# Kernel optimization log

Hardware: AMD Instinct MI355X
Metric: run time of the kernel (lower is better)

## Reference

```python
import jax, jax.numpy as jnp
import numpy as np

N_PARTICLES = 512
N_DIMS = 3
EPS_LJ = 1.0
RM = 1.0
ENERGY_FACTOR = 1.0
OSC_SCALE = 1.0
DIST_EPS = 1e-6  # bgflow distances_from_vectors eps inside sqrt


def setup_inputs() -> dict:
    key = jax.random.key(0)
    x = jax.random.normal(key, (128, N_PARTICLES * N_DIMS), dtype=jnp.float32)
    return {"x": x}


def reference(x):
    B = x.shape[0]
    xp = x.reshape(B, N_PARTICLES, N_DIMS)
    # all-pairs distance vectors r_ij = x_i - x_j  -> [B, N, N, D]
    diff = xp[:, :, None, :] - xp[:, None, :, :]
    r = jnp.sqrt(jnp.sum(diff * diff, axis=-1) + DIST_EPS)  # [B, N, N]
    eye = jnp.eye(N_PARTICLES, dtype=bool)
    # mask diagonal (bgflow removes self-pairs before the LJ energy)
    r_safe = jnp.where(eye, 1.0, r)
    inv6 = (RM / r_safe) ** 6
    lj = EPS_LJ * (inv6 * inv6 - 2.0 * inv6)
    lj = jnp.where(eye, 0.0, lj)
    lj_energies = lj.reshape(B, -1).sum(axis=-1) * ENERGY_FACTOR
    # harmonic oscillator term on mean-centered coordinates
    xc = xp - jnp.mean(xp, axis=1, keepdims=True)
    osc = 0.5 * jnp.sum(xc * xc, axis=(-2, -1))
    total = lj_energies + osc * OSC_SCALE
    return total[:, None]
```

## Files before the change

kernel.cpp:

```cpp
#include <hip/hip_runtime.h>

#define NP 512
#define BLOCK 512
#define JW 64
constexpr float DIST_EPS = 1e-6f;

__device__ __forceinline__ float waveSum(float v) {
    v += __shfl_down(v, 32, 64);
    v += __shfl_down(v, 16, 64);
    v += __shfl_down(v, 8, 64);
    v += __shfl_down(v, 4, 64);
    v += __shfl_down(v, 2, 64);
    v += __shfl_down(v, 1, 64);
    return v;
}

__global__ __launch_bounds__(BLOCK, 8) void lj_kernel(const float* __restrict__ x,
                                                      float* __restrict__ out) {
    const int b   = blockIdx.x >> 3;
    const int q   = blockIdx.x & 7;
    const int tid = threadIdx.x;
    const float* __restrict__ xb = x + b * (NP * 3);

    __shared__ __align__(16) float s[3 * NP];
    __shared__ float red[8 * 5];

    for (int g = tid; g < 3 * NP; g += BLOCK) {
        float v = xb[g];
        int p = g / 3;
        int d = g - p * 3;
        s[d * NP + p] = v;
    }
    __syncthreads();

    const float* sx = s;
    const float* sy = s + NP;
    const float* sz = s + 2 * NP;

    const int i     = tid;
    const int jbase = q * JW;

    const float xi = sx[i], yi = sy[i], zi = sz[i];

    float a0 = 0.f, a1 = 0.f, a2 = 0.f, a3 = 0.f;

    #pragma unroll 2
    for (int j = jbase; j < jbase + JW; j += 4) {
        float4 jx = *reinterpret_cast<const float4*>(sx + j);
        float4 jy = *reinterpret_cast<const float4*>(sy + j);
        float4 jz = *reinterpret_cast<const float4*>(sz + j);

        {
            float dx = xi - jx.x, dy = yi - jy.x, dz = zi - jz.x;
            float d2 = fmaf(dx, dx, fmaf(dy, dy, fmaf(dz, dz, DIST_EPS)));
            float d6 = d2 * d2 * d2;
            float i6 = __builtin_amdgcn_rcpf(d6);
            i6 = (j + 0 == i) ? 0.f : i6;
            a0 = fmaf(i6, i6 - 2.0f, a0);
        }
        {
            float dx = xi - jx.y, dy = yi - jy.y, dz = zi - jz.y;
            float d2 = fmaf(dx, dx, fmaf(dy, dy, fmaf(dz, dz, DIST_EPS)));
            float d6 = d2 * d2 * d2;
            float i6 = __builtin_amdgcn_rcpf(d6);
            i6 = (j + 1 == i) ? 0.f : i6;
            a1 = fmaf(i6, i6 - 2.0f, a1);
        }
        {
            float dx = xi - jx.z, dy = yi - jy.z, dz = zi - jz.z;
            float d2 = fmaf(dx, dx, fmaf(dy, dy, fmaf(dz, dz, DIST_EPS)));
            float d6 = d2 * d2 * d2;
            float i6 = __builtin_amdgcn_rcpf(d6);
            i6 = (j + 2 == i) ? 0.f : i6;
            a2 = fmaf(i6, i6 - 2.0f, a2);
        }
        {
            float dx = xi - jx.w, dy = yi - jy.w, dz = zi - jz.w;
            float d2 = fmaf(dx, dx, fmaf(dy, dy, fmaf(dz, dz, DIST_EPS)));
            float d6 = d2 * d2 * d2;
            float i6 = __builtin_amdgcn_rcpf(d6);
            i6 = (j + 3 == i) ? 0.f : i6;
            a3 = fmaf(i6, i6 - 2.0f, a3);
        }
    }
    float acc = (a0 + a1) + (a2 + a3);

    float sxs = 0.f, sys = 0.f, szs = 0.f, sqs = 0.f;
    if (q == 0) {
        float px = sx[tid], py = sy[tid], pz = sz[tid];
        sxs = px; sys = py; szs = pz;
        sqs = fmaf(px, px, fmaf(py, py, pz * pz));
    }

    const int wid  = tid >> 6;
    const int lane = tid & 63;
    float r0 = waveSum(acc);
    float r1 = waveSum(sxs);
    float r2 = waveSum(sys);
    float r3 = waveSum(szs);
    float r4 = waveSum(sqs);
    if (lane == 0) {
        red[wid * 5 + 0] = r0;
        red[wid * 5 + 1] = r1;
        red[wid * 5 + 2] = r2;
        red[wid * 5 + 3] = r3;
        red[wid * 5 + 4] = r4;
    }
    __syncthreads();
    if (tid == 0) {
        float t0 = 0.f, t1 = 0.f, t2 = 0.f, t3 = 0.f, t4 = 0.f;
        #pragma unroll
        for (int w = 0; w < 8; ++w) {
            t0 += red[w * 5 + 0];
            t1 += red[w * 5 + 1];
            t2 += red[w * 5 + 2];
            t3 += red[w * 5 + 3];
            t4 += red[w * 5 + 4];
        }
        float total = t0;
        if (q == 0) {
            float m2 = (t1 * t1 + t2 * t2 + t3 * t3) * (1.0f / NP);
            total += 0.5f * (t4 - m2);
        }
        atomicAdd(out + b, total);
    }
}

extern "C" void kernel_launch(void* const* d_in, const int* in_sizes, int n_in,
                              void* d_out, int out_size, void* d_ws, size_t ws_size,
                              hipStream_t stream) {
    const float* x = (const float*)d_in[0];
    float* out = (float*)d_out;
    const int B = in_sizes[0] / (NP * 3);
    lj_kernel<<<dim3(8 * B, 1, 1), BLOCK, 0, stream>>>(x, out);
}
```

Measured before the change: 65.08 us.

## Exploit pair symmetry to halve LJ pair evaluations via circular half-window

Uses the symmetry of the pair energy to compute each unordered pair once. Particle coordinates are duplicated into shared memory so each thread can walk a wrapped window of about half the particles, and the block sum is doubled. Boundary groups get special handling: a partial first group (j > i), and half weights on the antipodal group. The diagonal masks leave the inner loop, so the remaining arithmetic is roughly halved, at the cost of more shared memory, extra edge code, and uneven work across the q blocks.

```diff
diff --git a/kernel.cpp b/kernel.cpp
--- a/kernel.cpp
+++ b/kernel.cpp
@@ -2,7 +2,7 @@
 
 #define NP 512
 #define BLOCK 512
-#define JW 64
+#define NDUP 768
 constexpr float DIST_EPS = 1e-6f;
 
 __device__ __forceinline__ float waveSum(float v) {
@@ -22,30 +22,40 @@
     const int tid = threadIdx.x;
     const float* __restrict__ xb = x + b * (NP * 3);
 
-    __shared__ __align__(16) float s[3 * NP];
+    __shared__ __align__(16) float s[3 * NDUP];
     __shared__ float red[8 * 5];
 
     for (int g = tid; g < 3 * NP; g += BLOCK) {
         float v = xb[g];
         int p = g / 3;
         int d = g - p * 3;
-        s[d * NP + p] = v;
+        s[d * NDUP + p] = v;
+    }
+    for (int g = tid; g < 3 * 256; g += BLOCK) {
+        int d = g >> 8;
+        int p = g & 255;
+        s[d * NDUP + NP + p] = xb[p * 3 + d];
     }
     __syncthreads();
 
     const float* sx = s;
-    const float* sy = s + NP;
-    const float* sz = s + 2 * NP;
+    const float* sy = s + NDUP;
+    const float* sz = s + 2 * NDUP;
 
-    const int i     = tid;
-    const int jbase = q * JW;
+    const int i      = tid;
+    const int m      = i & 3;
+    const int jstart = i & ~3;
 
     const float xi = sx[i], yi = sy[i], zi = sz[i];
 
     float a0 = 0.f, a1 = 0.f, a2 = 0.f, a3 = 0.f;
 
+    const int gbeg = q * 8 + 1;
+    const int gend = (q == 7) ? 63 : q * 8 + 8;
+
     #pragma unroll 2
-    for (int j = jbase; j < jbase + JW; j += 4) {
+    for (int g = gbeg; g <= gend; ++g) {
+        const int j = jstart + 4 * g;
         float4 jx = *reinterpret_cast<const float4*>(sx + j);
         float4 jy = *reinterpret_cast<const float4*>(sy + j);
         float4 jz = *reinterpret_cast<const float4*>(sz + j);
@@ -55,7 +65,6 @@
             float d2 = fmaf(dx, dx, fmaf(dy, dy, fmaf(dz, dz, DIST_EPS)));
             float d6 = d2 * d2 * d2;
             float i6 = __builtin_amdgcn_rcpf(d6);
-            i6 = (j + 0 == i) ? 0.f : i6;
             a0 = fmaf(i6, i6 - 2.0f, a0);
         }
         {
@@ -63,7 +72,6 @@
             float d2 = fmaf(dx, dx, fmaf(dy, dy, fmaf(dz, dz, DIST_EPS)));
             float d6 = d2 * d2 * d2;
             float i6 = __builtin_amdgcn_rcpf(d6);
-            i6 = (j + 1 == i) ? 0.f : i6;
             a1 = fmaf(i6, i6 - 2.0f, a1);
         }
         {
@@ -71,7 +79,6 @@
             float d2 = fmaf(dx, dx, fmaf(dy, dy, fmaf(dz, dz, DIST_EPS)));
             float d6 = d2 * d2 * d2;
             float i6 = __builtin_amdgcn_rcpf(d6);
-            i6 = (j + 2 == i) ? 0.f : i6;
             a2 = fmaf(i6, i6 - 2.0f, a2);
         }
         {
@@ -79,11 +86,36 @@
             float d2 = fmaf(dx, dx, fmaf(dy, dy, fmaf(dz, dz, DIST_EPS)));
             float d6 = d2 * d2 * d2;
             float i6 = __builtin_amdgcn_rcpf(d6);
-            i6 = (j + 3 == i) ? 0.f : i6;
             a3 = fmaf(i6, i6 - 2.0f, a3);
         }
     }
     float acc = (a0 + a1) + (a2 + a3);
+
+    if (q == 0) {
+        #pragma unroll
+        for (int e = 0; e < 4; ++e) {
+            int j = jstart + e;
+            float dx = xi - sx[j], dy = yi - sy[j], dz = zi - sz[j];
+            float d2 = fmaf(dx, dx, fmaf(dy, dy, fmaf(dz, dz, DIST_EPS)));
+            float d6 = d2 * d2 * d2;
+            float i6 = __builtin_amdgcn_rcpf(d6);
+            float v = i6 * (i6 - 2.0f);
+            acc += (e > m) ? v : 0.f;
+        }
+    }
+    if (q == 7) {
+        #pragma unroll
+        for (int e = 0; e < 4; ++e) {
+            int j = jstart + 256 + e;
+            float dx = xi - sx[j], dy = yi - sy[j], dz = zi - sz[j];
+            float d2 = fmaf(dx, dx, fmaf(dy, dy, fmaf(dz, dz, DIST_EPS)));
+            float d6 = d2 * d2 * d2;
+            float i6 = __builtin_amdgcn_rcpf(d6);
+            float v = i6 * (i6 - 2.0f);
+            float w = (e < m) ? 1.0f : ((e == m) ? 0.5f : 0.0f);
+            acc = fmaf(w, v, acc);
+        }
+    }
 
     float sxs = 0.f, sys = 0.f, szs = 0.f, sqs = 0.f;
     if (q == 0) {
@@ -117,7 +149,7 @@
             t3 += red[w * 5 + 3];
             t4 += red[w * 5 + 4];
         }
-        float total = t0;
+        float total = 2.0f * t0;
         if (q == 0) {
             float m2 = (t1 * t1 + t2 * t2 + t3 * t3) * (1.0f / NP);
             total += 0.5f * (t4 - m2);
```

Result: faster. 60.98 us (-6.3%).
